# Performance work log

Hardware: AMD Instinct MI355X
Metric: run time of the kernel (lower is better)

The kernel has to match this reference:

```python
import jax, jax.numpy as jnp
import numpy as np

N = 100000          # num nodes
AVG_DEG = 16
E = N * AVG_DEG     # non-self-loop edges
D = 128             # in_dim == out_dim
H = 8               # heads
DH = D // H         # per-head dim
NEG_SLOPE = 0.2
EPS = 1e-5


def _layer_norm(h, g, b):
    mu = jnp.mean(h, axis=-1, keepdims=True)
    var = jnp.var(h, axis=-1, keepdims=True)
    return (h - mu) * jax.lax.rsqrt(var + EPS) * g + b


def setup_inputs() -> dict:
    key = jax.random.key(0)
    ks = jax.random.split(key, 12)
    x = jax.random.normal(ks[0], (N, D), dtype=jnp.float32)

    # edges with no self-loops, then append self-loops (mimics remove_self_loops + add_self_loops)
    rng = np.random.default_rng(0)
    src = rng.integers(0, N, size=E, dtype=np.int64)
    off = rng.integers(1, N, size=E, dtype=np.int64)
    dst = (src + off) % N
    loops = np.arange(N, dtype=np.int64)
    edge_index = jnp.asarray(
        np.stack([np.concatenate([src, loops]), np.concatenate([dst, loops])], axis=0))

    s = 0.02
    p = {
        'Wq': jax.random.normal(ks[1], (D, H * DH), jnp.float32) * s,
        'bq': jnp.zeros((H * DH,), jnp.float32),
        'Wk': jax.random.normal(ks[2], (D, H * DH), jnp.float32) * s,
        'bk': jnp.zeros((H * DH,), jnp.float32),
        'Wv': jax.random.normal(ks[3], (D, H * DH), jnp.float32) * s,
        'bv': jnp.zeros((H * DH,), jnp.float32),
        'Wo': jax.random.normal(ks[4], (D, D), jnp.float32) * s,
        'bo': jnp.zeros((D,), jnp.float32),
        'g1': jnp.ones((D,), jnp.float32),
        'b1': jnp.zeros((D,), jnp.float32),
        'Wf1': jax.random.normal(ks[5], (D, 2 * D), jnp.float32) * s,
        'bf1': jnp.zeros((2 * D,), jnp.float32),
        'Wf2': jax.random.normal(ks[6], (2 * D, D), jnp.float32) * s,
        'bf2': jnp.zeros((D,), jnp.float32),
        'g2': jnp.ones((D,), jnp.float32),
        'b2': jnp.zeros((D,), jnp.float32),
    }
    return {'x': x, 'edge_index': edge_index, **p}


def reference(x, edge_index, Wq, bq, Wk, bk, Wv, bv, Wo, bo, g1, b1,
              Wf1, bf1, Wf2, bf2, g2, b2):
    src, dst = edge_index[0], edge_index[1]

    Qh = (x @ Wq + bq).reshape(N, H, DH)
    Kh = (x @ Wk + bk).reshape(N, H, DH)
    Vh = (x @ Wv + bv).reshape(N, H, DH)

    # per-node scalar score per head: Q_n . K_n / sqrt(d_head)  -> [N, H]
    score = jnp.sum(Qh * Kh, axis=-1) / jnp.sqrt(jnp.float32(DH))

    # edge-wise: alpha = leaky_relu(score[src] + score[dst])  -> [Etot, H]
    alpha = jax.nn.leaky_relu(score[src] + score[dst], NEG_SLOPE)

    # segment softmax over destination nodes
    amax = jax.ops.segment_max(alpha, dst, num_segments=N)  # [N, H]
    ex = jnp.exp(alpha - amax[dst])
    denom = jax.ops.segment_sum(ex, dst, num_segments=N)
    alpha = ex / (denom[dst] + 1e-16)

    # weighted message aggregation: sum_j alpha_ij * V_j
    msg = Vh[src] * alpha[:, :, None]                        # [Etot, H, DH]
    out = jax.ops.segment_sum(msg, dst, num_segments=N)      # [N, H, DH]
    h = out.reshape(N, D)

    h = h @ Wo + bo
    h = h + x                       # residual 1
    h = _layer_norm(h, g1, b1)

    h2 = jax.nn.relu(h @ Wf1 + bf1)
    h2 = h2 @ Wf2 + bf2
    h = h2 + h                      # residual 2
    h = _layer_norm(h, g2, b2)
    return h
```

## Files before the change

kernel.cpp:

```cpp
#include <hip/hip_runtime.h>
#include <math.h>


#define GT_D 128

typedef short bf16x8 __attribute__((ext_vector_type(8)));
typedef float f32x4  __attribute__((ext_vector_type(4)));

union frag_u { bf16x8 v; ushort u[8]; };

__device__ __forceinline__ ushort f2bf(float f) {
    union { float f; unsigned u; } x; x.f = f;
    unsigned r = x.u + 0x7FFF + ((x.u >> 16) & 1);
    return (ushort)(r >> 16);
}

static inline char* align256(char* p) {
    return (char*)(((uintptr_t)p + 255) & ~(uintptr_t)255);
}

__global__ __launch_bounds__(256)
void ei_detect(const int* __restrict__ raw, int nOdd, int* __restrict__ flag)
{
    int i = blockIdx.x * 256 + threadIdx.x;
    int nz = 0;
    for (int j = i; j < nOdd; j += 256 * gridDim.x)
        nz |= (raw[2 * j + 1] != 0);
    if (nz) atomicOr(flag, 1);
}

__global__ __launch_bounds__(256)
void bucket_kernel(const int* __restrict__ raw, int Etot,
                   const int* __restrict__ flag,
                   int* __restrict__ deg, int* __restrict__ bucket)
{
    const int e = blockIdx.x * 256 + threadIdx.x;
    if (e >= Etot) return;
    const bool is64 = (*flag == 0);
    int s, d;
    if (is64) { s = raw[2 * e];  d = raw[2 * (Etot + e)]; }
    else      { s = raw[e];      d = raw[Etot + e]; }
    const int slot = atomicAdd(&deg[d], 1);
    if (slot < 64) bucket[(long)d * 64 + slot] = s;
}

__global__ __launch_bounds__(256)
void prep_qkv(const float* __restrict__ Wq, const float* __restrict__ Wk,
              const float* __restrict__ Wv, const float* __restrict__ bq,
              const float* __restrict__ bk, const float* __restrict__ bv,
              ushort* __restrict__ Wt, float* __restrict__ bias)
{
    const int i = blockIdx.x * 256 + threadIdx.x;
    if (i < 384 * 128) {
        const int n = i >> 7, k = i & 127;
        float v = (n < 128) ? Wq[k * 128 + n]
                : (n < 256) ? Wk[k * 128 + (n - 128)]
                            : Wv[k * 128 + (n - 256)];
        Wt[i] = f2bf(v);
    }
    if (i < 384)
        bias[i] = (i < 128) ? bq[i] : (i < 256) ? bk[i - 128] : bv[i - 256];
}

__global__ __launch_bounds__(256)
void prep_w(const float* __restrict__ W, ushort* __restrict__ Wt, int K, int N)
{
    const int i = blockIdx.x * 256 + threadIdx.x;
    if (i >= K * N) return;
    const int n = i / K, k = i - n * K;
    Wt[i] = f2bf(W[k * N + n]);
}

template<int MODE, bool AFP32>
__global__ __launch_bounds__(256)
void gemm_mfma(const void* __restrict__ Ap, int lda,
               const ushort* __restrict__ Wt, int K,
               const float* __restrict__ bias,
               const float* __restrict__ R, int ldr,
               void* __restrict__ Cp, int ldc, int M)
{
    const int w    = threadIdx.x >> 6;
    const int l    = threadIdx.x & 63;
    const int lr   = l & 15;
    const int lg   = l >> 4;
    const int row0 = blockIdx.x * 64 + w * 16;
    const int col0 = blockIdx.y * 128;

    const int arow  = row0 + lr;
    const long arowc = (arow < M) ? arow : (M - 1);

    f32x4 acc[8];
    #pragma unroll
    for (int ct = 0; ct < 8; ++ct) acc[ct] = (f32x4){0.f, 0.f, 0.f, 0.f};

    for (int k0 = 0; k0 < K; k0 += 32) {
        frag_u a;
        if (AFP32) {
            const float* A = (const float*)Ap;
            const float4 f0 = *(const float4*)&A[arowc * lda + k0 + lg * 8];
            const float4 f1 = *(const float4*)&A[arowc * lda + k0 + lg * 8 + 4];
            a.u[0] = f2bf(f0.x); a.u[1] = f2bf(f0.y);
            a.u[2] = f2bf(f0.z); a.u[3] = f2bf(f0.w);
            a.u[4] = f2bf(f1.x); a.u[5] = f2bf(f1.y);
            a.u[6] = f2bf(f1.z); a.u[7] = f2bf(f1.w);
        } else {
            const ushort* A = (const ushort*)Ap;
            a.v = *(const bf16x8*)&A[arowc * lda + k0 + lg * 8];
        }
        #pragma unroll
        for (int ct = 0; ct < 8; ++ct) {
            const bf16x8 b =
                *(const bf16x8*)&Wt[(long)(col0 + ct * 16 + lr) * K + k0 + lg * 8];
            acc[ct] = __builtin_amdgcn_mfma_f32_16x16x32_bf16(a.v, b, acc[ct], 0, 0, 0);
        }
    }

    #pragma unroll
    for (int ct = 0; ct < 8; ++ct) {
        const int col  = col0 + ct * 16 + lr;
        const float bv = bias[col];
        #pragma unroll
        for (int r = 0; r < 4; ++r) {
            const int row = row0 + lg * 4 + r;
            if (row >= M) continue;
            float v = acc[ct][r] + bv;
            if (MODE == 1) {
                v = v > 0.f ? v : 0.f;
                ((ushort*)Cp)[(long)row * ldc + col] = f2bf(v);
            } else {
                if (MODE == 2) v += R[(long)row * ldr + col];
                ((float*)Cp)[(long)row * ldc + col] = v;
            }
        }
    }
}

__global__ __launch_bounds__(256)
void score_kernel(const float* __restrict__ QKV, float* __restrict__ score, int n)
{
    const int i = blockIdx.x * 256 + threadIdx.x;
    if (i >= n) return;
    const int node = i >> 3, h = i & 7;
    const float4* q = (const float4*)(QKV + (long)node * 384 + h * 16);
    const float4* k = (const float4*)(QKV + (long)node * 384 + 128 + h * 16);
    float s = 0.f;
    #pragma unroll
    for (int j = 0; j < 4; ++j) {
        const float4 qv = q[j], kv = k[j];
        s += qv.x * kv.x + qv.y * kv.y + qv.z * kv.z + qv.w * kv.w;
    }
    score[i] = s * 0.25f;
}

__global__ __launch_bounds__(256)
void aggregate_kernel(const float* __restrict__ QKV,
                      const float* __restrict__ score,
                      const int* __restrict__ deg,
                      const int* __restrict__ bucket,
                      ushort* __restrict__ att, int n)
{
    const int grp = threadIdx.x >> 5;
    const int l   = threadIdx.x & 31;
    const int d   = blockIdx.x * 8 + grp;
    if (d >= n) return;
    const int head   = l >> 2;
    const float sdst = score[(long)d * 8 + head];
    int dg = deg[d]; if (dg > 64) dg = 64;
    float psum = 0.f;
    float4 acc = make_float4(0.f, 0.f, 0.f, 0.f);
    for (int j = 0; j < dg; ++j) {
        const int s = bucket[(long)d * 64 + j];
        float a = score[(long)s * 8 + head] + sdst;
        a = a > 0.f ? a : 0.2f * a;
        const float p = __expf(a);
        psum += p;
        const float4 v = *(const float4*)&QKV[(long)s * 384 + 256 + l * 4];
        acc.x += p * v.x; acc.y += p * v.y; acc.z += p * v.z; acc.w += p * v.w;
    }
    const float rinv = 1.0f / (psum + 1e-16f);
    ushort4 o;
    o.x = f2bf(acc.x * rinv); o.y = f2bf(acc.y * rinv);
    o.z = f2bf(acc.z * rinv); o.w = f2bf(acc.w * rinv);
    *(ushort4*)&att[(long)d * 768 + l * 4] = o;
}

__global__ __launch_bounds__(256)
void ln_kernel(const float* __restrict__ X, int ldx,
               const float* __restrict__ g, const float* __restrict__ b,
               float* __restrict__ outF, int ldo,
               ushort* __restrict__ outB, int ldob, int M)
{
    const int wave = threadIdx.x >> 6;
    const int lane = threadIdx.x & 63;
    const int row  = blockIdx.x * 4 + wave;
    if (row >= M) return;
    const float2 v = *(const float2*)&X[(long)row * ldx + lane * 2];
    float s = v.x + v.y;
    #pragma unroll
    for (int off = 32; off > 0; off >>= 1) s += __shfl_xor(s, off);
    const float mu = s * (1.0f / 128.0f);
    const float dx = v.x - mu, dy = v.y - mu;
    float q = dx * dx + dy * dy;
    #pragma unroll
    for (int off = 32; off > 0; off >>= 1) q += __shfl_xor(q, off);
    const float rstd = rsqrtf(q * (1.0f / 128.0f) + 1e-5f);
    const float2 gg = *(const float2*)&g[lane * 2];
    const float2 bb = *(const float2*)&b[lane * 2];
    float2 o;
    o.x = dx * rstd * gg.x + bb.x;
    o.y = dy * rstd * gg.y + bb.y;
    *(float2*)&outF[(long)row * ldo + lane * 2] = o;
    if (outB) {
        ushort2 ob; ob.x = f2bf(o.x); ob.y = f2bf(o.y);
        *(ushort2*)&outB[(long)row * ldob + lane * 2] = ob;
    }
}

extern "C" void kernel_launch(void* const* d_in, const int* in_sizes, int n_in,
                              void* d_out, int out_size, void* d_ws, size_t ws_size,
                              hipStream_t stream)
{
    const float* x   = (const float*)d_in[0];
    const int*   ei  = (const int*)d_in[1];
    const float* Wq  = (const float*)d_in[2];
    const float* bq  = (const float*)d_in[3];
    const float* Wk  = (const float*)d_in[4];
    const float* bk  = (const float*)d_in[5];
    const float* Wv  = (const float*)d_in[6];
    const float* bv  = (const float*)d_in[7];
    const float* Wo  = (const float*)d_in[8];
    const float* bo  = (const float*)d_in[9];
    const float* g1  = (const float*)d_in[10];
    const float* b1  = (const float*)d_in[11];
    const float* Wf1 = (const float*)d_in[12];
    const float* bf1 = (const float*)d_in[13];
    const float* Wf2 = (const float*)d_in[14];
    const float* bf2 = (const float*)d_in[15];
    const float* g2  = (const float*)d_in[16];
    const float* b2  = (const float*)d_in[17];
    float* out = (float*)d_out;

    const int N    = in_sizes[0] / GT_D;
    const int Etot = in_sizes[1] / 2;

    char* w = (char*)d_ws;
    char* big0 = w;                    w = align256(w + (size_t)N * 384 * sizeof(float));
    float*  sc    = (float*)w;         w = align256(w + (size_t)N * 8 * sizeof(float));
    int*    deg   = (int*)w;           w = align256(w + (size_t)N * sizeof(int));
    int*    flag  = (int*)w;           w = align256(w + 256);
    int*    bkt   = (int*)w;           w = align256(w + (size_t)N * 64 * sizeof(int));
    ushort* wqkvt = (ushort*)w;        w = align256(w + (size_t)384 * 128 * sizeof(ushort));
    float*  bqkv  = (float*)w;         w = align256(w + 384 * sizeof(float));
    ushort* wot   = (ushort*)w;        w = align256(w + (size_t)128 * 128 * sizeof(ushort));
    ushort* wf1t  = (ushort*)w;        w = align256(w + (size_t)256 * 128 * sizeof(ushort));
    ushort* wf2t  = (ushort*)w;        w = align256(w + (size_t)128 * 256 * sizeof(ushort));

    float*  QKV  = (float*)big0;
    ushort* att  = (ushort*)big0;
    float*  hp   = (float*)big0 + 256;
    float*  h1   = (float*)big0 + 128;
    ushort* h1b  = (ushort*)big0 + 512;
    ushort* hid  = (ushort*)big0;

    const dim3 blk(256);
    const int mblk = (N + 63) / 64;

    hipMemsetAsync(flag, 0, sizeof(int), stream);
    hipMemsetAsync(deg, 0, (size_t)N * sizeof(int), stream);
    ei_detect<<<dim3(512), blk, 0, stream>>>(ei, Etot, flag);
    bucket_kernel<<<dim3((Etot + 255) / 256), blk, 0, stream>>>(ei, Etot, flag, deg, bkt);

    prep_qkv<<<dim3(192), blk, 0, stream>>>(Wq, Wk, Wv, bq, bk, bv, wqkvt, bqkv);
    prep_w<<<dim3(64),  blk, 0, stream>>>(Wo,  wot,  128, 128);
    prep_w<<<dim3(128), blk, 0, stream>>>(Wf1, wf1t, 128, 256);
    prep_w<<<dim3(128), blk, 0, stream>>>(Wf2, wf2t, 256, 128);

    gemm_mfma<0, true><<<dim3(mblk, 3), blk, 0, stream>>>(
        x, 128, wqkvt, 128, bqkv, nullptr, 0, QKV, 384, N);

    score_kernel<<<dim3((N * 8 + 255) / 256), blk, 0, stream>>>(QKV, sc, N * 8);

    aggregate_kernel<<<dim3((N + 7) / 8), blk, 0, stream>>>(QKV, sc, deg, bkt, att, N);

    gemm_mfma<2, false><<<dim3(mblk, 1), blk, 0, stream>>>(
        att, 768, wot, 128, bo, x, 128, hp, 384, N);

    ln_kernel<<<dim3((N + 3) / 4), blk, 0, stream>>>(hp, 384, g1, b1, h1, 384, h1b, 768, N);

    gemm_mfma<1, false><<<dim3(mblk, 2), blk, 0, stream>>>(
        h1b, 768, wf1t, 128, bf1, nullptr, 0, hid, 768, N);

    gemm_mfma<2, false><<<dim3(mblk, 1), blk, 0, stream>>>(
        hid, 768, wf2t, 256, bf2, h1, 384, out, 128, N);

    ln_kernel<<<dim3((N + 3) / 4), blk, 0, stream>>>(out, 128, g2, b2, out, 128, nullptr, 0, N);
}
```

Baseline: 804.1 us.

## Fuse score into QKV GEMM, store V as bf16, compact workspace buffers

The QKV GEMM now computes all 384 columns in one block and reduces Q·K per head in registers with shuffles, writing scores directly. Q and K are no longer stored and V is written as bf16, so the score kernel is removed. The aggregate kernel then gathers half-width V rows, and the workspace is laid out more compactly. The costs are larger register pressure (24 accumulators) and bf16 rounding of V.

```diff
diff --git a/kernel.cpp b/kernel.cpp
--- a/kernel.cpp
+++ b/kernel.cpp
@@ -13,6 +13,9 @@
     union { float f; unsigned u; } x; x.f = f;
     unsigned r = x.u + 0x7FFF + ((x.u >> 16) & 1);
     return (ushort)(r >> 16);
+}
+__device__ __forceinline__ float bf2f(ushort u) {
+    union { unsigned u; float f; } x; x.u = ((unsigned)u) << 16; return x.f;
 }
 
 static inline char* align256(char* p) {
@@ -71,27 +74,27 @@
     Wt[i] = f2bf(W[k * N + n]);
 }
 
-template<int MODE, bool AFP32>
+template<int MODE, bool AFP32, int CT>
 __global__ __launch_bounds__(256)
 void gemm_mfma(const void* __restrict__ Ap, int lda,
                const ushort* __restrict__ Wt, int K,
                const float* __restrict__ bias,
                const float* __restrict__ R, int ldr,
-               void* __restrict__ Cp, int ldc, int M)
+               void* __restrict__ Cp, int ldc, int M,
+               float* __restrict__ scOut)
 {
     const int w    = threadIdx.x >> 6;
     const int l    = threadIdx.x & 63;
     const int lr   = l & 15;
     const int lg   = l >> 4;
     const int row0 = blockIdx.x * 64 + w * 16;
-    const int col0 = blockIdx.y * 128;
-
-    const int arow  = row0 + lr;
+
+    const int  arow  = row0 + lr;
     const long arowc = (arow < M) ? arow : (M - 1);
 
-    f32x4 acc[8];
-    #pragma unroll
-    for (int ct = 0; ct < 8; ++ct) acc[ct] = (f32x4){0.f, 0.f, 0.f, 0.f};
+    f32x4 acc[CT];
+    #pragma unroll
+    for (int ct = 0; ct < CT; ++ct) acc[ct] = (f32x4){0.f, 0.f, 0.f, 0.f};
 
     for (int k0 = 0; k0 < K; k0 += 32) {
         frag_u a;
@@ -108,27 +111,58 @@
             a.v = *(const bf16x8*)&A[arowc * lda + k0 + lg * 8];
         }
         #pragma unroll
-        for (int ct = 0; ct < 8; ++ct) {
-            const bf16x8 b =
-                *(const bf16x8*)&Wt[(long)(col0 + ct * 16 + lr) * K + k0 + lg * 8];
+        for (int ct = 0; ct < CT; ++ct) {
+            const bf16x8 b = *(const bf16x8*)&Wt[(long)(ct * 16 + lr) * K + k0 + lg * 8];
             acc[ct] = __builtin_amdgcn_mfma_f32_16x16x32_bf16(a.v, b, acc[ct], 0, 0, 0);
         }
     }
 
     #pragma unroll
-    for (int ct = 0; ct < 8; ++ct) {
-        const int col  = col0 + ct * 16 + lr;
-        const float bv = bias[col];
+    for (int ct = 0; ct < CT; ++ct) {
+        const float bv = bias[ct * 16 + lr];
+        #pragma unroll
+        for (int r = 0; r < 4; ++r) acc[ct][r] += bv;
+    }
+
+    if (MODE == 0) {
+        #pragma unroll
+        for (int h = 0; h < 8; ++h) {
+            #pragma unroll
+            for (int r = 0; r < 4; ++r) {
+                float p = acc[h][r] * acc[h + 8][r];
+                p += __shfl_xor(p, 1);
+                p += __shfl_xor(p, 2);
+                p += __shfl_xor(p, 4);
+                p += __shfl_xor(p, 8);
+                const int row = row0 + lg * 4 + r;
+                if (lr == h && row < M) scOut[(long)row * 8 + h] = p * 0.25f;
+            }
+        }
+        #pragma unroll
+        for (int ct = 16; ct < 24; ++ct) {
+            const int col = (ct - 16) * 16 + lr;
+            #pragma unroll
+            for (int r = 0; r < 4; ++r) {
+                const int row = row0 + lg * 4 + r;
+                if (row < M) ((ushort*)Cp)[(long)row * ldc + col] = f2bf(acc[ct][r]);
+            }
+        }
+        return;
+    }
+
+    #pragma unroll
+    for (int ct = 0; ct < CT; ++ct) {
+        const int col = ct * 16 + lr;
         #pragma unroll
         for (int r = 0; r < 4; ++r) {
             const int row = row0 + lg * 4 + r;
             if (row >= M) continue;
-            float v = acc[ct][r] + bv;
+            float v = acc[ct][r];
             if (MODE == 1) {
                 v = v > 0.f ? v : 0.f;
                 ((ushort*)Cp)[(long)row * ldc + col] = f2bf(v);
             } else {
-                if (MODE == 2) v += R[(long)row * ldr + col];
+                v += R[(long)row * ldr + col];
                 ((float*)Cp)[(long)row * ldc + col] = v;
             }
         }
@@ -136,28 +170,11 @@
 }
 
 __global__ __launch_bounds__(256)
-void score_kernel(const float* __restrict__ QKV, float* __restrict__ score, int n)
-{
-    const int i = blockIdx.x * 256 + threadIdx.x;
-    if (i >= n) return;
-    const int node = i >> 3, h = i & 7;
-    const float4* q = (const float4*)(QKV + (long)node * 384 + h * 16);
-    const float4* k = (const float4*)(QKV + (long)node * 384 + 128 + h * 16);
-    float s = 0.f;
-    #pragma unroll
-    for (int j = 0; j < 4; ++j) {
-        const float4 qv = q[j], kv = k[j];
-        s += qv.x * kv.x + qv.y * kv.y + qv.z * kv.z + qv.w * kv.w;
-    }
-    score[i] = s * 0.25f;
-}
-
-__global__ __launch_bounds__(256)
-void aggregate_kernel(const float* __restrict__ QKV,
+void aggregate_kernel(const ushort* __restrict__ Z,
                       const float* __restrict__ score,
                       const int* __restrict__ deg,
                       const int* __restrict__ bucket,
-                      ushort* __restrict__ att, int n)
+                      int n)
 {
     const int grp = threadIdx.x >> 5;
     const int l   = threadIdx.x & 31;
@@ -174,14 +191,15 @@
         a = a > 0.f ? a : 0.2f * a;
         const float p = __expf(a);
         psum += p;
-        const float4 v = *(const float4*)&QKV[(long)s * 384 + 256 + l * 4];
-        acc.x += p * v.x; acc.y += p * v.y; acc.z += p * v.z; acc.w += p * v.w;
+        const ushort4 v = *(const ushort4*)&Z[(long)s * 256 + l * 4];
+        acc.x += p * bf2f(v.x); acc.y += p * bf2f(v.y);
+        acc.z += p * bf2f(v.z); acc.w += p * bf2f(v.w);
     }
     const float rinv = 1.0f / (psum + 1e-16f);
     ushort4 o;
     o.x = f2bf(acc.x * rinv); o.y = f2bf(acc.y * rinv);
     o.z = f2bf(acc.z * rinv); o.w = f2bf(acc.w * rinv);
-    *(ushort4*)&att[(long)d * 768 + l * 4] = o;
+    *(ushort4*)&((ushort*)Z)[(long)d * 256 + 128 + l * 4] = o;
 }
 
 __global__ __launch_bounds__(256)
@@ -244,23 +262,21 @@
     const int Etot = in_sizes[1] / 2;
 
     char* w = (char*)d_ws;
-    char* big0 = w;                    w = align256(w + (size_t)N * 384 * sizeof(float));
-    float*  sc    = (float*)w;         w = align256(w + (size_t)N * 8 * sizeof(float));
-    int*    deg   = (int*)w;           w = align256(w + (size_t)N * sizeof(int));
-    int*    flag  = (int*)w;           w = align256(w + 256);
-    int*    bkt   = (int*)w;           w = align256(w + (size_t)N * 64 * sizeof(int));
-    ushort* wqkvt = (ushort*)w;        w = align256(w + (size_t)384 * 128 * sizeof(ushort));
-    float*  bqkv  = (float*)w;         w = align256(w + 384 * sizeof(float));
-    ushort* wot   = (ushort*)w;        w = align256(w + (size_t)128 * 128 * sizeof(ushort));
-    ushort* wf1t  = (ushort*)w;        w = align256(w + (size_t)256 * 128 * sizeof(ushort));
-    ushort* wf2t  = (ushort*)w;        w = align256(w + (size_t)128 * 256 * sizeof(ushort));
-
-    float*  QKV  = (float*)big0;
-    ushort* att  = (ushort*)big0;
-    float*  hp   = (float*)big0 + 256;
-    float*  h1   = (float*)big0 + 128;
-    ushort* h1b  = (ushort*)big0 + 512;
-    ushort* hid  = (ushort*)big0;
+    ushort* Z     = (ushort*)w;  w = align256(w + (size_t)N * 256 * sizeof(ushort));
+    float*  hp    = (float*)w;   w = align256(w + (size_t)N * 128 * sizeof(float));
+    ushort* h1b   = (ushort*)w;  w = align256(w + (size_t)N * 128 * sizeof(ushort));
+    float*  sc    = (float*)w;   w = align256(w + (size_t)N * 8 * sizeof(float));
+    int*    deg   = (int*)w;     w = align256(w + (size_t)N * sizeof(int));
+    int*    flag  = (int*)w;     w = align256(w + 256);
+    int*    bkt   = (int*)w;     w = align256(w + (size_t)N * 64 * sizeof(int));
+    ushort* wqkvt = (ushort*)w;  w = align256(w + (size_t)384 * 128 * sizeof(ushort));
+    float*  bqkv  = (float*)w;   w = align256(w + 384 * sizeof(float));
+    ushort* wot   = (ushort*)w;  w = align256(w + (size_t)128 * 128 * sizeof(ushort));
+    ushort* wf1t  = (ushort*)w;  w = align256(w + (size_t)256 * 128 * sizeof(ushort));
+    ushort* wf2t  = (ushort*)w;  w = align256(w + (size_t)128 * 256 * sizeof(ushort));
+    float*  h1    = hp;
+    ushort* att   = Z + 128;
+    ushort* hid   = Z;
 
     const dim3 blk(256);
     const int mblk = (N + 63) / 64;
@@ -275,23 +291,21 @@
     prep_w<<<dim3(128), blk, 0, stream>>>(Wf1, wf1t, 128, 256);
     prep_w<<<dim3(128), blk, 0, stream>>>(Wf2, wf2t, 256, 128);
 
-    gemm_mfma<0, true><<<dim3(mblk, 3), blk, 0, stream>>>(
-        x, 128, wqkvt, 128, bqkv, nullptr, 0, QKV, 384, N);
-
-    score_kernel<<<dim3((N * 8 + 255) / 256), blk, 0, stream>>>(QKV, sc, N * 8);
-
-    aggregate_kernel<<<dim3((N + 7) / 8), blk, 0, stream>>>(QKV, sc, deg, bkt, att, N);
-
-    gemm_mfma<2, false><<<dim3(mblk, 1), blk, 0, stream>>>(
-        att, 768, wot, 128, bo, x, 128, hp, 384, N);
-
-    ln_kernel<<<dim3((N + 3) / 4), blk, 0, stream>>>(hp, 384, g1, b1, h1, 384, h1b, 768, N);
-
-    gemm_mfma<1, false><<<dim3(mblk, 2), blk, 0, stream>>>(
-        h1b, 768, wf1t, 128, bf1, nullptr, 0, hid, 768, N);
-
-    gemm_mfma<2, false><<<dim3(mblk, 1), blk, 0, stream>>>(
-        hid, 768, wf2t, 256, bf2, h1, 384, out, 128, N);
+    gemm_mfma<0, true, 24><<<dim3(mblk), blk, 0, stream>>>(
+        x, 128, wqkvt, 128, bqkv, nullptr, 0, Z, 256, N, sc);
+
+    aggregate_kernel<<<dim3((N + 7) / 8), blk, 0, stream>>>(Z, sc, deg, bkt, N);
+
+    gemm_mfma<2, false, 8><<<dim3(mblk), blk, 0, stream>>>(
+        att, 256, wot, 128, bo, x, 128, hp, 128, N, nullptr);
+
+    ln_kernel<<<dim3((N + 3) / 4), blk, 0, stream>>>(hp, 128, g1, b1, h1, 128, h1b, 128, N);
+
+    gemm_mfma<1, false, 16><<<dim3(mblk), blk, 0, stream>>>(
+        h1b, 128, wf1t, 128, bf1, nullptr, 0, hid, 256, N, nullptr);
+
+    gemm_mfma<2, false, 8><<<dim3(mblk), blk, 0, stream>>>(
+        hid, 256, wf2t, 256, bf2, h1, 128, out, 128, N, nullptr);
 
     ln_kernel<<<dim3((N + 3) / 4), blk, 0, stream>>>(out, 128, g2, b2, out, 128, nullptr, 0, N);
 }
```

Result: faster. 769.0 us (-4.4%).
